# Performance work log

Measured on AMD Instinct MI355X. Metric: run time of the kernel, lower is better.

The kernel has to match this reference:

```python
import jax, jax.numpy as jnp
import numpy as np

N_ITERS = 3   # Routing default n_iters
EPS = 1e-5    # variance floor added to sig2
LN_EPS = 1e-5 # torch LayerNorm eps


def _routing(a_inp, mu_inp, W, Bias, beta_use, beta_ign):
    """Heinsen routing (gaussian p_model).
    a_inp: [b, n_i]; mu_inp: [b, n_i, c, d_inp]
    W: [1 or n_i, n_o, d_inp, d_out]; Bias: [n_o, c, d_out]; betas: [n_o].
    """
    if W.shape[0] == 1:  # weights shared across input capsules (n_inp not fixed)
        V = jnp.einsum('jdh,bicd->bijch', W[0], mu_inp) + Bias
    else:
        V = jnp.einsum('ijdh,bicd->bijch', W, mu_inp) + Bias
    n_out = V.shape[2]
    fa = jax.nn.sigmoid(a_inp)[..., None]          # [b, n_i, 1]
    R = jnp.full(V.shape[:3], 1.0 / n_out, dtype=V.dtype)
    a_out = mu_out = sig2 = Vm2 = None
    for it in range(N_ITERS):
        # E-step
        if it > 0:
            log_p = (-jnp.einsum('bijch,bjch->bij', Vm2, 1.0 / (2.0 * sig2))
                     - 0.5 * jnp.log(sig2).sum(axis=(-2, -1))[:, None, :])
            R = jax.nn.softmax(jax.nn.log_sigmoid(a_out)[:, None, :] + log_p, axis=-1)
        # D-step
        D_use = fa * R                              # [b, n_i, n_o]
        D_sum = D_use.sum(axis=-2)                  # [b, n_o]
        # M-step
        a_out = beta_use * D_sum - beta_ign * (fa.sum(axis=-2) - D_sum)
        nR = D_use / D_sum[:, None, :]
        mu_out = jnp.einsum('bij,bijch->bjch', nR, V)
        Vm2 = jnp.square(V - mu_out[:, None])
        sig2 = jnp.einsum('bij,bijch->bjch', nR, Vm2) + EPS
    return a_out, mu_out, sig2


def setup_inputs() -> dict:
    B, T = 32, 128
    d_depth, d_emb, d_cap, n_parts, n_classes = 13, 1024, 16, 64, 5
    key = jax.random.key(0)
    ks = jax.random.split(key, 8)
    mask = jax.random.uniform(ks[0], (B, T), jnp.float32, 0.05, 0.95)  # in (0,1) so logit is finite
    embs = jax.random.normal(ks[1], (B, T, d_depth, d_emb), jnp.float32)
    depth_emb = jax.random.normal(ks[2], (d_depth, d_emb), jnp.float32) * 0.02
    ln_w = jnp.ones((d_emb,), jnp.float32)
    ln_b = jnp.zeros((d_emb,), jnp.float32)
    dp_w = jax.random.normal(ks[3], (n_parts, d_emb), jnp.float32) * np.sqrt(2.0 / d_emb)  # kaiming
    dp_b = jnp.zeros((n_parts,), jnp.float32)
    # Routing 1: d_cov=1, d_inp=n_parts, d_out=d_cap, n_out=n_parts, n_inp shared (-1)
    W1 = jax.random.normal(ks[4], (1, n_parts, n_parts, d_cap), jnp.float32) / n_parts
    B1 = jnp.zeros((n_parts, 1, d_cap), jnp.float32)
    bu1 = jnp.zeros((n_parts,), jnp.float32)
    bi1 = jnp.zeros((n_parts,), jnp.float32)
    # Routing 2: d_cov=1, d_inp=d_cap, d_out=d_cap, n_out=n_classes, n_inp=n_parts
    W2 = jax.random.normal(ks[5], (n_parts, n_classes, d_cap, d_cap), jnp.float32) / d_cap
    B2 = jnp.zeros((n_classes, 1, d_cap), jnp.float32)
    bu2 = jnp.zeros((n_classes,), jnp.float32)
    bi2 = jnp.zeros((n_classes,), jnp.float32)
    return dict(mask=mask, embs=embs, depth_emb=depth_emb, ln_w=ln_w, ln_b=ln_b,
                dp_w=dp_w, dp_b=dp_b, W1=W1, B1=B1, bu1=bu1, bi1=bi1,
                W2=W2, B2=B2, bu2=bu2, bi2=bi2)


def reference(mask, embs, depth_emb, ln_w, ln_b, dp_w, dp_b,
              W1, B1, bu1, bi1, W2, B2, bu2, bi2):
    B = mask.shape[0]
    d_depth = embs.shape[-2]
    # input activations: logit(mask), repeated over depth
    a = jnp.log(mask / (1.0 - mask))                       # [B, T]
    a = jnp.broadcast_to(a[..., None], a.shape + (d_depth,)).reshape(B, -1)  # [B, T*d_depth]
    # detect_parts: LayerNorm -> Linear -> Swish
    x = embs + depth_emb
    m = x.mean(axis=-1, keepdims=True)
    v = ((x - m) ** 2).mean(axis=-1, keepdims=True)        # biased var (torch LayerNorm)
    xn = (x - m) * jax.lax.rsqrt(v + LN_EPS) * ln_w + ln_b
    h = jnp.einsum('btde,pe->btdp', xn, dp_w) + dp_b
    mu = h * jax.nn.sigmoid(h)                             # Swish
    mu = mu.reshape(B, -1, 1, mu.shape[-1])                # [B, T*d_depth, 1, n_parts]
    a, mu, sig2 = _routing(a, mu, W1, B1, bu1, bi1)
    a, mu, sig2 = _routing(a, mu, W2, B2, bu2, bi2)
    return a, mu, sig2
```

## Files before the change

kernel.cpp:

```cpp
#include <hip/hip_runtime.h>
#include <hip/hip_bf16.h>

constexpr int BQ = 32;
constexpr int TT = 128;
constexpr int DD = 13;
constexpr int E  = 1024;
constexpr int P  = 64;
constexpr int C  = 16;
constexpr int NC = 5;
constexpr int NI = TT * DD;
constexpr int NROWS = BQ * NI;
constexpr int RB = 16;

__global__ void k_sumfa(const float* __restrict__ mask, float* __restrict__ sumfa)
{
    const int b = blockIdx.x, tid = threadIdx.x;
    float v = mask[b * TT + tid];
#pragma unroll
    for (int off = 32; off > 0; off >>= 1) v += __shfl_xor(v, off);
    __shared__ float p2[2];
    if ((tid & 63) == 0) p2[tid >> 6] = v;
    __syncthreads();
    if (tid == 0) sumfa[b] = (float)DD * (p2[0] + p2[1]);
}

__global__ __launch_bounds__(256) void
k1_parts_v(const float* __restrict__ embs, const float* __restrict__ depth_emb,
           const float* __restrict__ ln_w, const float* __restrict__ ln_b,
           const float* __restrict__ dp_w, const float* __restrict__ dp_b,
           const float* __restrict__ W1,  const float* __restrict__ B1,
           float* __restrict__ V)
{
    __shared__ float xn[RB][E];
    __shared__ float muL[RB][P];
    const int tid = threadIdx.x;
    const int wave = tid >> 6, lane = tid & 63;
    const int row0 = blockIdx.x * RB;

    for (int rr = 0; rr < 4; ++rr) {
        const int r = wave * 4 + rr;
        const int row = row0 + r;
        const int dd = row % DD;
        const float* xr = embs + (size_t)row * E;
        const float* de = depth_emb + (size_t)dd * E;
        float4 xv[4];
        float s = 0.f;
#pragma unroll
        for (int k = 0; k < 4; ++k) {
            const int e = 4 * lane + 256 * k;
            float4 a = *reinterpret_cast<const float4*>(xr + e);
            const float4 d4 = *reinterpret_cast<const float4*>(de + e);
            a.x += d4.x; a.y += d4.y; a.z += d4.z; a.w += d4.w;
            xv[k] = a;
            s += a.x + a.y + a.z + a.w;
        }
#pragma unroll
        for (int off = 32; off > 0; off >>= 1) s += __shfl_xor(s, off);
        const float mean = s * (1.f / E);
        float vs = 0.f;
#pragma unroll
        for (int k = 0; k < 4; ++k) {
            const float4 a = xv[k];
            const float dx = a.x - mean, dy = a.y - mean, dz = a.z - mean, dw = a.w - mean;
            vs += dx * dx + dy * dy + dz * dz + dw * dw;
        }
#pragma unroll
        for (int off = 32; off > 0; off >>= 1) vs += __shfl_xor(vs, off);
        const float rstd = rsqrtf(vs * (1.f / E) + 1e-5f);
#pragma unroll
        for (int k = 0; k < 4; ++k) {
            const int e = 4 * lane + 256 * k;
            const float4 a = xv[k];
            const float4 w4 = *reinterpret_cast<const float4*>(ln_w + e);
            const float4 b4 = *reinterpret_cast<const float4*>(ln_b + e);
            float4 o4;
            o4.x = (a.x - mean) * rstd * w4.x + b4.x;
            o4.y = (a.y - mean) * rstd * w4.y + b4.y;
            o4.z = (a.z - mean) * rstd * w4.z + b4.z;
            o4.w = (a.w - mean) * rstd * w4.w + b4.w;
            *reinterpret_cast<float4*>(&xn[r][e]) = o4;
        }
    }
    __syncthreads();

    {
        const int pg = tid >> 4, eq = tid & 15;
        float acc[4][RB];
#pragma unroll
        for (int q = 0; q < 4; ++q)
#pragma unroll
            for (int r = 0; r < RB; ++r) acc[q][r] = 0.f;

        for (int kk = 0; kk < 16; ++kk) {
            const int e = kk * 64 + eq * 4;
            float4 w4[4];
#pragma unroll
            for (int q = 0; q < 4; ++q)
                w4[q] = *reinterpret_cast<const float4*>(dp_w + (size_t)(pg + q * 16) * E + e);
#pragma unroll
            for (int r = 0; r < RB; ++r) {
                const float4 x4 = *reinterpret_cast<const float4*>(&xn[r][e]);
#pragma unroll
                for (int q = 0; q < 4; ++q) {
                    acc[q][r] = fmaf(w4[q].x, x4.x, acc[q][r]);
                    acc[q][r] = fmaf(w4[q].y, x4.y, acc[q][r]);
                    acc[q][r] = fmaf(w4[q].z, x4.z, acc[q][r]);
                    acc[q][r] = fmaf(w4[q].w, x4.w, acc[q][r]);
                }
            }
        }
#pragma unroll
        for (int q = 0; q < 4; ++q)
#pragma unroll
            for (int r = 0; r < RB; ++r) {
                float v = acc[q][r];
                v += __shfl_xor(v, 1);
                v += __shfl_xor(v, 2);
                v += __shfl_xor(v, 4);
                v += __shfl_xor(v, 8);
                acc[q][r] = v;
            }
        if (eq == 0) {
#pragma unroll
            for (int q = 0; q < 4; ++q) {
                const int p = pg + q * 16;
                const float bb = dp_b[p];
#pragma unroll
                for (int r = 0; r < RB; ++r) {
                    const float h = acc[q][r] + bb;
                    muL[r][p] = h / (1.f + __expf(-h));
                }
            }
        }
    }
    __syncthreads();

    {
        const int h0 = wave * 4;
        const int j = lane;
        float4 acc[RB];
        const float4 b4 = *reinterpret_cast<const float4*>(B1 + j * C + h0);
#pragma unroll
        for (int r = 0; r < RB; ++r) acc[r] = b4;
        const float* w1p = W1 + (size_t)j * P * C + h0;
        for (int d = 0; d < P; ++d) {
            const float4 w4 = *reinterpret_cast<const float4*>(w1p + (size_t)d * C);
#pragma unroll
            for (int r = 0; r < RB; ++r) {
                const float m = muL[r][d];
                acc[r].x = fmaf(m, w4.x, acc[r].x);
                acc[r].y = fmaf(m, w4.y, acc[r].y);
                acc[r].z = fmaf(m, w4.z, acc[r].z);
                acc[r].w = fmaf(m, w4.w, acc[r].w);
            }
        }
#pragma unroll
        for (int r = 0; r < RB; ++r) {
            const size_t row = (size_t)(row0 + r);
            float* vp = V + (row * C + h0) * (size_t)P + j;
            vp[0 * P] = acc[r].x;
            vp[1 * P] = acc[r].y;
            vp[2 * P] = acc[r].z;
            vp[3 * P] = acc[r].w;
        }
    }
}

__global__ __launch_bounds__(256) void
k2_pass(const float* __restrict__ V, const float* __restrict__ mask,
        const float* __restrict__ c1v, const float* __restrict__ ivv,
        const float* __restrict__ c0v, float* __restrict__ Smu,
        float* __restrict__ SV2, float* __restrict__ Dsum, const int it)
{
    __shared__ float lacc[P][34];
    const int tid = threadIdx.x;
    const int wave = tid >> 6, j = tid & 63;
    const int b = blockIdx.x / (NI / 64);
    const int tile = blockIdx.x % (NI / 64);

    for (int k = tid; k < P * 34; k += 256) (&lacc[0][0])[k] = 0.f;

    float c1[16], iv[16], c0 = 0.f;
    if (it > 0) {
        const float4* cp = reinterpret_cast<const float4*>(c1v + ((size_t)b * P + j) * C);
        const float4* ip = reinterpret_cast<const float4*>(ivv + ((size_t)b * P + j) * C);
#pragma unroll
        for (int k = 0; k < 4; ++k) {
            const float4 c4 = cp[k]; const float4 i4 = ip[k];
            c1[k * 4 + 0] = c4.x; c1[k * 4 + 1] = c4.y; c1[k * 4 + 2] = c4.z; c1[k * 4 + 3] = c4.w;
            iv[k * 4 + 0] = i4.x; iv[k * 4 + 1] = i4.y; iv[k * 4 + 2] = i4.z; iv[k * 4 + 3] = i4.w;
        }
        c0 = c0v[(size_t)b * P + j];
    }

    const int i0 = tile * 64 + wave * 16;
    const float* vb = V + ((size_t)(b * NI + i0) * C) * P + j;

    float dsum = 0.f;
    float smuA[16], sv2A[16];
#pragma unroll
    for (int h = 0; h < 16; ++h) { smuA[h] = 0.f; sv2A[h] = 0.f; }

    __syncthreads();

    float va[2][16];
#pragma unroll
    for (int h = 0; h < 16; ++h) va[0][h] = vb[(size_t)h * P];

#pragma unroll
    for (int s = 0; s < 16; ++s) {
        const int cb = s & 1;
        if (s < 15) {
#pragma unroll
            for (int h = 0; h < 16; ++h)
                va[cb ^ 1][h] = vb[(size_t)((s + 1) * C + h) * P];
        }
        float R;
        if (it > 0) {
            float q = c0;
#pragma unroll
            for (int h = 0; h < 16; ++h) {
                const float v = va[cb][h];
                q = fmaf(v, fmaf(-v, iv[h], c1[h]), q);
            }
            float m = q;
#pragma unroll
            for (int off = 32; off > 0; off >>= 1) m = fmaxf(m, __shfl_xor(m, off));
            const float e = __expf(q - m);
            float sum = e;
#pragma unroll
            for (int off = 32; off > 0; off >>= 1) sum += __shfl_xor(sum, off);
            R = e / sum;
        } else {
            R = 1.f / 64.f;
        }
        const int i = i0 + s;
        const float fa = mask[b * TT + i / DD];
        const float w = fa * R;
        dsum += w;
#pragma unroll
        for (int h = 0; h < 16; ++h) {
            const float v = va[cb][h];
            smuA[h] = fmaf(w, v, smuA[h]);
            sv2A[h] = fmaf(w * v, v, sv2A[h]);
        }
    }

#pragma unroll
    for (int h = 0; h < 16; ++h) {
        atomicAdd(&lacc[j][h], smuA[h]);
        atomicAdd(&lacc[j][16 + h], sv2A[h]);
    }
    atomicAdd(&lacc[j][32], dsum);
    __syncthreads();

    for (int k = tid; k < P * 33; k += 256) {
        const int jj = k / 33, r = k % 33;
        const float v = lacc[jj][r];
        if (r < 16)      atomicAdd(&Smu[((size_t)b * P + jj) * C + r], v);
        else if (r < 32) atomicAdd(&SV2[((size_t)b * P + jj) * C + (r - 16)], v);
        else             atomicAdd(&Dsum[(size_t)b * P + jj], v);
    }
}

__global__ void k2f(const float* __restrict__ Smu, const float* __restrict__ SV2,
                    const float* __restrict__ Dsum, const float* __restrict__ sumfa,
                    const float* __restrict__ bu, const float* __restrict__ bi,
                    float* __restrict__ muo, float* __restrict__ ivv,
                    float* __restrict__ c1v, float* __restrict__ c0v,
                    float* __restrict__ a1)
{
    const int t = blockIdx.x * blockDim.x + threadIdx.x;
    if (t >= BQ * P) return;
    const int b = t / P, j = t % P;
    const float ds = Dsum[t];
    const float inv = 1.f / ds;
    const float ao = bu[j] * ds - bi[j] * (sumfa[b] - ds);
    a1[t] = ao;
    const float lsg = (ao < 0.f) ? (ao - log1pf(__expf(ao))) : (-log1pf(__expf(-ao)));
    float sumlog = 0.f, moiv = 0.f;
#pragma unroll
    for (int h = 0; h < C; ++h) {
        const float m = Smu[t * C + h] * inv;
        const float s2 = fmaxf(SV2[t * C + h] * inv - m * m, 0.f) + 1e-5f;
        const float iv = 0.5f / s2;
        muo[t * C + h] = m;
        ivv[t * C + h] = iv;
        c1v[t * C + h] = 2.f * m * iv;
        sumlog += logf(s2);
        moiv += m * m * iv;
    }
    c0v[t] = lsg - 0.5f * sumlog - moiv;
}

__global__ void k3_routing2(const float* __restrict__ muo, const float* __restrict__ a1,
                            const float* __restrict__ W2, const float* __restrict__ B2,
                            const float* __restrict__ bu2, const float* __restrict__ bi2,
                            float* __restrict__ out)
{
    __shared__ float mu1L[P][C];
    __shared__ float faL[P];
    __shared__ float V2L[P][NC][C];
    __shared__ float RL[P][NC];
    __shared__ float mu2L[NC][C];
    __shared__ float s2L[NC][C];
    __shared__ float isL[NC][C];
    __shared__ float dsL[NC];
    __shared__ float biasL[NC];
    __shared__ float a2L[NC];
    __shared__ float sumfa2s;
    const int b = blockIdx.x, tid = threadIdx.x;

    for (int k = tid; k < P * C; k += 256) (&mu1L[0][0])[k] = muo[(size_t)b * P * C + k];
    if (tid < P) {
        const float a = a1[(size_t)b * P + tid];
        faL[tid] = 1.f / (1.f + __expf(-a));
    }
    __syncthreads();
    if (tid == 0) {
        float s = 0.f;
        for (int i = 0; i < P; ++i) s += faL[i];
        sumfa2s = s;
    }
    {
        const int i = tid >> 2, hq = tid & 3;
        for (int jj = 0; jj < NC; ++jj) {
            float4 acc = *reinterpret_cast<const float4*>(B2 + jj * C + hq * 4);
            const float* wp = W2 + ((size_t)(i * NC + jj) * C) * C + hq * 4;
#pragma unroll
            for (int d = 0; d < C; ++d) {
                const float m = mu1L[i][d];
                const float4 w4 = *reinterpret_cast<const float4*>(wp + d * C);
                acc.x += m * w4.x; acc.y += m * w4.y; acc.z += m * w4.z; acc.w += m * w4.w;
            }
            *reinterpret_cast<float4*>(&V2L[i][jj][hq * 4]) = acc;
        }
    }
    __syncthreads();

    for (int it = 0; it < 3; ++it) {
        if (tid < P) {
            const int i = tid;
            if (it == 0) {
#pragma unroll
                for (int jj = 0; jj < NC; ++jj) RL[i][jj] = 1.f / NC;
            } else {
                float sc[NC];
                float m = -3.4e38f;
#pragma unroll
                for (int jj = 0; jj < NC; ++jj) {
                    float q = 0.f;
#pragma unroll
                    for (int h = 0; h < C; ++h) {
                        const float d = V2L[i][jj][h] - mu2L[jj][h];
                        q += d * d * isL[jj][h];
                    }
                    sc[jj] = biasL[jj] - q;
                    m = fmaxf(m, sc[jj]);
                }
                float sum = 0.f;
#pragma unroll
                for (int jj = 0; jj < NC; ++jj) { sc[jj] = __expf(sc[jj] - m); sum += sc[jj]; }
                const float invs = 1.f / sum;
#pragma unroll
                for (int jj = 0; jj < NC; ++jj) RL[i][jj] = sc[jj] * invs;
            }
        }
        __syncthreads();
        if (tid < NC) {
            float ds = 0.f;
            for (int i = 0; i < P; ++i) ds += faL[i] * RL[i][tid];
            dsL[tid] = ds;
        }
        __syncthreads();
        if (tid < NC * C) {
            const int jj = tid / C, h = tid % C;
            float smu = 0.f, sv2 = 0.f;
            for (int i = 0; i < P; ++i) {
                const float w = faL[i] * RL[i][jj];
                const float v = V2L[i][jj][h];
                smu += w * v;
                sv2 += w * v * v;
            }
            const float inv = 1.f / dsL[jj];
            const float m = smu * inv;
            const float s2 = fmaxf(sv2 * inv - m * m, 0.f) + 1e-5f;
            mu2L[jj][h] = m;
            s2L[jj][h] = s2;
            isL[jj][h] = 0.5f / s2;
        }
        __syncthreads();
        if (tid < NC) {
            const float ds = dsL[tid];
            const float ao = bu2[tid] * ds - bi2[tid] * (sumfa2s - ds);
            a2L[tid] = ao;
            const float lsg = (ao < 0.f) ? (ao - log1pf(__expf(ao))) : (-log1pf(__expf(-ao)));
            float sl = 0.f;
#pragma unroll
            for (int h = 0; h < C; ++h) sl += logf(s2L[tid][h]);
            biasL[tid] = lsg - 0.5f * sl;
        }
        __syncthreads();
    }

    if (tid < NC) out[(size_t)b * NC + tid] = a2L[tid];
    if (tid < NC * C) {
        const int jj = tid / C, h = tid % C;
        out[BQ * NC + ((size_t)b * NC + jj) * C + h] = mu2L[jj][h];
        out[BQ * NC + BQ * NC * C + ((size_t)b * NC + jj) * C + h] = s2L[jj][h];
    }
}

extern "C" void kernel_launch(void* const* d_in, const int* in_sizes, int n_in,
                              void* d_out, int out_size, void* d_ws, size_t ws_size,
                              hipStream_t stream)
{
    (void)in_sizes; (void)n_in; (void)out_size; (void)ws_size;
    const float* mask      = (const float*)d_in[0];
    const float* embs      = (const float*)d_in[1];
    const float* depth_emb = (const float*)d_in[2];
    const float* ln_w      = (const float*)d_in[3];
    const float* ln_b      = (const float*)d_in[4];
    const float* dp_w      = (const float*)d_in[5];
    const float* dp_b      = (const float*)d_in[6];
    const float* W1        = (const float*)d_in[7];
    const float* B1        = (const float*)d_in[8];
    const float* bu1       = (const float*)d_in[9];
    const float* bi1       = (const float*)d_in[10];
    const float* W2        = (const float*)d_in[11];
    const float* B2        = (const float*)d_in[12];
    const float* bu2       = (const float*)d_in[13];
    const float* bi2       = (const float*)d_in[14];
    float* out = (float*)d_out;

    float* ws = (float*)d_ws;
    size_t o = 0;
    float* V     = ws + o; o += (size_t)NROWS * P * C;
    float* Smu   = ws + o; o += (size_t)BQ * P * C;
    float* SV2   = ws + o; o += (size_t)BQ * P * C;
    float* Dsum  = ws + o; o += (size_t)BQ * P;
    float* muo   = ws + o; o += (size_t)BQ * P * C;
    float* ivv   = ws + o; o += (size_t)BQ * P * C;
    float* c1v   = ws + o; o += (size_t)BQ * P * C;
    float* c0v   = ws + o; o += (size_t)BQ * P;
    float* a1    = ws + o; o += (size_t)BQ * P;
    float* sumfa = ws + o; o += (size_t)BQ;

    k_sumfa<<<BQ, 128, 0, stream>>>(mask, sumfa);
    k1_parts_v<<<NROWS / RB, 256, 0, stream>>>(embs, depth_emb, ln_w, ln_b,
                                               dp_w, dp_b, W1, B1, V);
    for (int it = 0; it < 3; ++it) {
        hipMemsetAsync(Smu, 0, (size_t)(2 * BQ * P * C + BQ * P) * sizeof(float), stream);
        k2_pass<<<BQ * (NI / 64), 256, 0, stream>>>(V, mask, c1v, ivv, c0v,
                                                    Smu, SV2, Dsum, it);
        k2f<<<(BQ * P) / 256, 256, 0, stream>>>(Smu, SV2, Dsum, sumfa, bu1, bi1,
                                                muo, ivv, c1v, c0v, a1);
    }
    k3_routing2<<<BQ, 256, 0, stream>>>(muo, a1, W2, B2, bu2, bi2, out);
}
```

Before: 931.4 us.

## Fold LayerNorm into projection weights and re-layout V as row-major [row][j][h]

Precomputes LayerNorm-folded projection weights, depth-embedding dot products and moment terms in a prep kernel. The parts projection can then run directly on raw embs, one thread per row, with mean and variance recovered algebraically. V is now stored in a [row][j*16+h] layout: k1b computes it as a dense GEMM with a transposed W1, and the k2 pass reads contiguous float4s per thread. The per-iteration memset is replaced by zeroing the accumulators in k2f. The one-row-per-thread GEMM reads wext from cache with high register pressure, and computing variance as E[x²]-mean² carries cancellation risk.

```diff
diff --git a/kernel.cpp b/kernel.cpp
--- a/kernel.cpp
+++ b/kernel.cpp
@@ -10,7 +10,7 @@
 constexpr int NC = 5;
 constexpr int NI = TT * DD;
 constexpr int NROWS = BQ * NI;
-constexpr int RB = 16;
+constexpr int NCOL = 80;
 
 __global__ void k_sumfa(const float* __restrict__ mask, float* __restrict__ sumfa)
 {
@@ -24,146 +24,188 @@
     if (tid == 0) sumfa[b] = (float)DD * (p2[0] + p2[1]);
 }
 
+__global__ void k0_pre(const float* __restrict__ ln_w, const float* __restrict__ ln_b,
+                       const float* __restrict__ dp_w, const float* __restrict__ dp_b,
+                       const float* __restrict__ depth_emb, const float* __restrict__ W1,
+                       float* __restrict__ wext, float* __restrict__ W1m,
+                       float* __restrict__ c1t, float* __restrict__ c2t,
+                       float* __restrict__ dwt, float* __restrict__ sde1,
+                       float* __restrict__ sde2)
+{
+    const int blk = blockIdx.x, tid = threadIdx.x;
+    if (blk < 64) {
+        __shared__ float red[15][256];
+        const int p = blk;
+        float accv[15];
+#pragma unroll
+        for (int c = 0; c < 15; ++c) accv[c] = 0.f;
+        for (int k = tid; k < E; k += 256) {
+            const float w = dp_w[(size_t)p * E + k];
+            const float gw = ln_w[k] * w;
+            accv[0] += gw;
+            accv[1] += ln_b[k] * w;
+#pragma unroll
+            for (int d = 0; d < 13; ++d) accv[2 + d] += depth_emb[(size_t)d * E + k] * gw;
+        }
+#pragma unroll
+        for (int c = 0; c < 15; ++c) red[c][tid] = accv[c];
+        __syncthreads();
+        if (tid < 15) {
+            float s = 0.f;
+            for (int t = 0; t < 256; ++t) s += red[tid][t];
+            if (tid == 0)      c1t[p] = s;
+            else if (tid == 1) c2t[p] = s + dp_b[p];
+            else               dwt[(tid - 2) * 64 + p] = s;
+        }
+    } else if (blk < 77) {
+        __shared__ float red[2][256];
+        const int d = blk - 64;
+        float s1 = 0.f, s2 = 0.f;
+        for (int k = tid; k < E; k += 256) {
+            const float v = depth_emb[(size_t)d * E + k];
+            s1 += v; s2 += v * v;
+        }
+        red[0][tid] = s1; red[1][tid] = s2;
+        __syncthreads();
+        if (tid < 2) {
+            float s = 0.f;
+            for (int t = 0; t < 256; ++t) s += red[tid][t];
+            if (tid == 0) sde1[d] = s; else sde2[d] = s;
+        }
+    } else if (blk < 77 + 320) {
+        const int idx = (blk - 77) * 256 + tid;
+        const int k = idx / NCOL, c = idx % NCOL;
+        float v = 0.f;
+        if (c < 64)      v = ln_w[k] * dp_w[(size_t)c * E + k];
+        else if (c < 77) v = depth_emb[(size_t)(c - 64) * E + k];
+        wext[idx] = v;
+    } else {
+        const int t = (blk - 397) * 256 + tid;
+        const int d = t >> 10, col = t & 1023, j = col >> 4, h = col & 15;
+        W1m[t] = W1[((size_t)j * 64 + d) * 16 + h];
+    }
+}
+
 __global__ __launch_bounds__(256) void
-k1_parts_v(const float* __restrict__ embs, const float* __restrict__ depth_emb,
-           const float* __restrict__ ln_w, const float* __restrict__ ln_b,
-           const float* __restrict__ dp_w, const float* __restrict__ dp_b,
-           const float* __restrict__ W1,  const float* __restrict__ B1,
-           float* __restrict__ V)
-{
-    __shared__ float xn[RB][E];
-    __shared__ float muL[RB][P];
+k1a(const float* __restrict__ embs, const float* __restrict__ wext,
+    const float* __restrict__ c1t, const float* __restrict__ c2t,
+    const float* __restrict__ dwt, const float* __restrict__ sde1,
+    const float* __restrict__ sde2, float* __restrict__ V)
+{
+    const int row = blockIdx.x * 256 + threadIdx.x;
+    const float* xr = embs + (size_t)row * E;
+    float4 acc[20];
+#pragma unroll
+    for (int c = 0; c < 20; ++c) acc[c] = make_float4(0.f, 0.f, 0.f, 0.f);
+    float s = 0.f, s2 = 0.f;
+
+    for (int k0 = 0; k0 < E; k0 += 32) {
+        float4 xb[8];
+#pragma unroll
+        for (int q = 0; q < 8; ++q)
+            xb[q] = *reinterpret_cast<const float4*>(xr + k0 + q * 4);
+#pragma unroll
+        for (int q = 0; q < 8; ++q) {
+            const float x0 = xb[q].x, x1 = xb[q].y, x2 = xb[q].z, x3 = xb[q].w;
+            const float* wr = wext + (size_t)(k0 + q * 4) * NCOL;
+#pragma unroll
+            for (int c = 0; c < 20; ++c) {
+                const float4 w0 = *reinterpret_cast<const float4*>(wr + c * 4);
+                const float4 w1 = *reinterpret_cast<const float4*>(wr + NCOL + c * 4);
+                const float4 w2 = *reinterpret_cast<const float4*>(wr + 2 * NCOL + c * 4);
+                const float4 w3 = *reinterpret_cast<const float4*>(wr + 3 * NCOL + c * 4);
+                acc[c].x = fmaf(x0, w0.x, fmaf(x1, w1.x, fmaf(x2, w2.x, fmaf(x3, w3.x, acc[c].x))));
+                acc[c].y = fmaf(x0, w0.y, fmaf(x1, w1.y, fmaf(x2, w2.y, fmaf(x3, w3.y, acc[c].y))));
+                acc[c].z = fmaf(x0, w0.z, fmaf(x1, w1.z, fmaf(x2, w2.z, fmaf(x3, w3.z, acc[c].z))));
+                acc[c].w = fmaf(x0, w0.w, fmaf(x1, w1.w, fmaf(x2, w2.w, fmaf(x3, w3.w, acc[c].w))));
+            }
+            s += x0 + x1 + x2 + x3;
+            s2 = fmaf(x0, x0, fmaf(x1, x1, fmaf(x2, x2, fmaf(x3, x3, s2))));
+        }
+    }
+
+    const int d = row % DD;
+    float deD = 0.f;
+#pragma unroll
+    for (int dd = 0; dd < 13; ++dd) {
+        const int ci = (64 + dd) >> 2, mi = (64 + dd) & 3;
+        const float v = (mi == 0) ? acc[ci].x : (mi == 1) ? acc[ci].y : (mi == 2) ? acc[ci].z : acc[ci].w;
+        if (dd == d) deD = v;
+    }
+    const float mean = (s + sde1[d]) * (1.f / E);
+    const float var = (s2 + 2.f * deD + sde2[d]) * (1.f / E) - mean * mean;
+    const float rstd = rsqrtf(var + 1e-5f);
+    const float* dwr = dwt + d * 64;
+    float* mup = V + (size_t)row * 1024 + 960;
+#pragma unroll
+    for (int c = 0; c < 16; ++c) {
+        const float4 ed = acc[c];
+        const float4 dv = *reinterpret_cast<const float4*>(dwr + c * 4);
+        const float4 cv1 = *reinterpret_cast<const float4*>(c1t + c * 4);
+        const float4 cv2 = *reinterpret_cast<const float4*>(c2t + c * 4);
+        float4 h, mu;
+        h.x = fmaf(rstd, ed.x + dv.x - mean * cv1.x, cv2.x);
+        h.y = fmaf(rstd, ed.y + dv.y - mean * cv1.y, cv2.y);
+        h.z = fmaf(rstd, ed.z + dv.z - mean * cv1.z, cv2.z);
+        h.w = fmaf(rstd, ed.w + dv.w - mean * cv1.w, cv2.w);
+        mu.x = h.x / (1.f + __expf(-h.x));
+        mu.y = h.y / (1.f + __expf(-h.y));
+        mu.z = h.z / (1.f + __expf(-h.z));
+        mu.w = h.w / (1.f + __expf(-h.w));
+        *reinterpret_cast<float4*>(mup + c * 4) = mu;
+    }
+}
+
+__global__ __launch_bounds__(256) void
+k1b(const float* __restrict__ W1m, const float* __restrict__ B1, float* __restrict__ V)
+{
+    __shared__ float muL[16][64];
     const int tid = threadIdx.x;
-    const int wave = tid >> 6, lane = tid & 63;
-    const int row0 = blockIdx.x * RB;
-
-    for (int rr = 0; rr < 4; ++rr) {
-        const int r = wave * 4 + rr;
-        const int row = row0 + r;
-        const int dd = row % DD;
-        const float* xr = embs + (size_t)row * E;
-        const float* de = depth_emb + (size_t)dd * E;
-        float4 xv[4];
-        float s = 0.f;
-#pragma unroll
-        for (int k = 0; k < 4; ++k) {
-            const int e = 4 * lane + 256 * k;
-            float4 a = *reinterpret_cast<const float4*>(xr + e);
-            const float4 d4 = *reinterpret_cast<const float4*>(de + e);
-            a.x += d4.x; a.y += d4.y; a.z += d4.z; a.w += d4.w;
-            xv[k] = a;
-            s += a.x + a.y + a.z + a.w;
-        }
-#pragma unroll
-        for (int off = 32; off > 0; off >>= 1) s += __shfl_xor(s, off);
-        const float mean = s * (1.f / E);
-        float vs = 0.f;
-#pragma unroll
-        for (int k = 0; k < 4; ++k) {
-            const float4 a = xv[k];
-            const float dx = a.x - mean, dy = a.y - mean, dz = a.z - mean, dw = a.w - mean;
-            vs += dx * dx + dy * dy + dz * dz + dw * dw;
-        }
-#pragma unroll
-        for (int off = 32; off > 0; off >>= 1) vs += __shfl_xor(vs, off);
-        const float rstd = rsqrtf(vs * (1.f / E) + 1e-5f);
-#pragma unroll
-        for (int k = 0; k < 4; ++k) {
-            const int e = 4 * lane + 256 * k;
-            const float4 a = xv[k];
-            const float4 w4 = *reinterpret_cast<const float4*>(ln_w + e);
-            const float4 b4 = *reinterpret_cast<const float4*>(ln_b + e);
-            float4 o4;
-            o4.x = (a.x - mean) * rstd * w4.x + b4.x;
-            o4.y = (a.y - mean) * rstd * w4.y + b4.y;
-            o4.z = (a.z - mean) * rstd * w4.z + b4.z;
-            o4.w = (a.w - mean) * rstd * w4.w + b4.w;
-            *reinterpret_cast<float4*>(&xn[r][e]) = o4;
-        }
+    const int row0 = blockIdx.x * 16;
+#pragma unroll
+    for (int q = 0; q < 4; ++q) {
+        const int idx = q * 256 + tid;
+        muL[idx >> 6][idx & 63] = V[(size_t)(row0 + (idx >> 6)) * 1024 + 960 + (idx & 63)];
     }
     __syncthreads();
-
-    {
-        const int pg = tid >> 4, eq = tid & 15;
-        float acc[4][RB];
-#pragma unroll
-        for (int q = 0; q < 4; ++q)
-#pragma unroll
-            for (int r = 0; r < RB; ++r) acc[q][r] = 0.f;
-
-        for (int kk = 0; kk < 16; ++kk) {
-            const int e = kk * 64 + eq * 4;
-            float4 w4[4];
-#pragma unroll
-            for (int q = 0; q < 4; ++q)
-                w4[q] = *reinterpret_cast<const float4*>(dp_w + (size_t)(pg + q * 16) * E + e);
-#pragma unroll
-            for (int r = 0; r < RB; ++r) {
-                const float4 x4 = *reinterpret_cast<const float4*>(&xn[r][e]);
-#pragma unroll
-                for (int q = 0; q < 4; ++q) {
-                    acc[q][r] = fmaf(w4[q].x, x4.x, acc[q][r]);
-                    acc[q][r] = fmaf(w4[q].y, x4.y, acc[q][r]);
-                    acc[q][r] = fmaf(w4[q].z, x4.z, acc[q][r]);
-                    acc[q][r] = fmaf(w4[q].w, x4.w, acc[q][r]);
-                }
-            }
-        }
-#pragma unroll
-        for (int q = 0; q < 4; ++q)
-#pragma unroll
-            for (int r = 0; r < RB; ++r) {
-                float v = acc[q][r];
-                v += __shfl_xor(v, 1);
-                v += __shfl_xor(v, 2);
-                v += __shfl_xor(v, 4);
-                v += __shfl_xor(v, 8);
-                acc[q][r] = v;
-            }
-        if (eq == 0) {
-#pragma unroll
-            for (int q = 0; q < 4; ++q) {
-                const int p = pg + q * 16;
-                const float bb = dp_b[p];
-#pragma unroll
-                for (int r = 0; r < RB; ++r) {
-                    const float h = acc[q][r] + bb;
-                    muL[r][p] = h / (1.f + __expf(-h));
-                }
-            }
-        }
-    }
-    __syncthreads();
-
-    {
-        const int h0 = wave * 4;
-        const int j = lane;
-        float4 acc[RB];
-        const float4 b4 = *reinterpret_cast<const float4*>(B1 + j * C + h0);
-#pragma unroll
-        for (int r = 0; r < RB; ++r) acc[r] = b4;
-        const float* w1p = W1 + (size_t)j * P * C + h0;
-        for (int d = 0; d < P; ++d) {
-            const float4 w4 = *reinterpret_cast<const float4*>(w1p + (size_t)d * C);
-#pragma unroll
-            for (int r = 0; r < RB; ++r) {
-                const float m = muL[r][d];
-                acc[r].x = fmaf(m, w4.x, acc[r].x);
-                acc[r].y = fmaf(m, w4.y, acc[r].y);
-                acc[r].z = fmaf(m, w4.z, acc[r].z);
-                acc[r].w = fmaf(m, w4.w, acc[r].w);
-            }
-        }
-#pragma unroll
-        for (int r = 0; r < RB; ++r) {
-            const size_t row = (size_t)(row0 + r);
-            float* vp = V + (row * C + h0) * (size_t)P + j;
-            vp[0 * P] = acc[r].x;
-            vp[1 * P] = acc[r].y;
-            vp[2 * P] = acc[r].z;
-            vp[3 * P] = acc[r].w;
-        }
-    }
+    const int c4 = tid;
+    float4 acc[16];
+    const float4 bv = *reinterpret_cast<const float4*>(B1 + c4 * 4);
+#pragma unroll
+    for (int r = 0; r < 16; ++r) acc[r] = bv;
+
+    for (int kc = 0; kc < 64; kc += 8) {
+        float4 wreg[8];
+#pragma unroll
+        for (int kk = 0; kk < 8; ++kk)
+            wreg[kk] = *reinterpret_cast<const float4*>(W1m + (size_t)(kc + kk) * 1024 + c4 * 4);
+#pragma unroll
+        for (int r = 0; r < 16; ++r) {
+            const float4 ma = *reinterpret_cast<const float4*>(&muL[r][kc]);
+            const float4 mb = *reinterpret_cast<const float4*>(&muL[r][kc + 4]);
+            float4 a = acc[r];
+            a.x = fmaf(ma.x, wreg[0].x, a.x); a.y = fmaf(ma.x, wreg[0].y, a.y);
+            a.z = fmaf(ma.x, wreg[0].z, a.z); a.w = fmaf(ma.x, wreg[0].w, a.w);
+            a.x = fmaf(ma.y, wreg[1].x, a.x); a.y = fmaf(ma.y, wreg[1].y, a.y);
+            a.z = fmaf(ma.y, wreg[1].z, a.z); a.w = fmaf(ma.y, wreg[1].w, a.w);
+            a.x = fmaf(ma.z, wreg[2].x, a.x); a.y = fmaf(ma.z, wreg[2].y, a.y);
+            a.z = fmaf(ma.z, wreg[2].z, a.z); a.w = fmaf(ma.z, wreg[2].w, a.w);
+            a.x = fmaf(ma.w, wreg[3].x, a.x); a.y = fmaf(ma.w, wreg[3].y, a.y);
+            a.z = fmaf(ma.w, wreg[3].z, a.z); a.w = fmaf(ma.w, wreg[3].w, a.w);
+            a.x = fmaf(mb.x, wreg[4].x, a.x); a.y = fmaf(mb.x, wreg[4].y, a.y);
+            a.z = fmaf(mb.x, wreg[4].z, a.z); a.w = fmaf(mb.x, wreg[4].w, a.w);
+            a.x = fmaf(mb.y, wreg[5].x, a.x); a.y = fmaf(mb.y, wreg[5].y, a.y);
+            a.z = fmaf(mb.y, wreg[5].z, a.z); a.w = fmaf(mb.y, wreg[5].w, a.w);
+            a.x = fmaf(mb.z, wreg[6].x, a.x); a.y = fmaf(mb.z, wreg[6].y, a.y);
+            a.z = fmaf(mb.z, wreg[6].z, a.z); a.w = fmaf(mb.z, wreg[6].w, a.w);
+            a.x = fmaf(mb.w, wreg[7].x, a.x); a.y = fmaf(mb.w, wreg[7].y, a.y);
+            a.z = fmaf(mb.w, wreg[7].z, a.z); a.w = fmaf(mb.w, wreg[7].w, a.w);
+            acc[r] = a;
+        }
+    }
+#pragma unroll
+    for (int r = 0; r < 16; ++r)
+        *reinterpret_cast<float4*>(V + (size_t)(row0 + r) * 1024 + c4 * 4) = acc[r];
 }
 
 __global__ __launch_bounds__(256) void
@@ -173,84 +215,124 @@
         float* __restrict__ SV2, float* __restrict__ Dsum, const int it)
 {
     __shared__ float lacc[P][34];
-    const int tid = threadIdx.x;
-    const int wave = tid >> 6, j = tid & 63;
+    const int tid = threadIdx.x, wave = tid >> 6, j = tid & 63;
     const int b = blockIdx.x / (NI / 64);
     const int tile = blockIdx.x % (NI / 64);
-
     for (int k = tid; k < P * 34; k += 256) (&lacc[0][0])[k] = 0.f;
 
-    float c1[16], iv[16], c0 = 0.f;
+    float4 C1a, C1b, C1c, C1d, IVa, IVb, IVc, IVd;
+    float c0 = 0.f;
+    C1a = C1b = C1c = C1d = IVa = IVb = IVc = IVd = make_float4(0.f, 0.f, 0.f, 0.f);
     if (it > 0) {
         const float4* cp = reinterpret_cast<const float4*>(c1v + ((size_t)b * P + j) * C);
         const float4* ip = reinterpret_cast<const float4*>(ivv + ((size_t)b * P + j) * C);
-#pragma unroll
-        for (int k = 0; k < 4; ++k) {
-            const float4 c4 = cp[k]; const float4 i4 = ip[k];
-            c1[k * 4 + 0] = c4.x; c1[k * 4 + 1] = c4.y; c1[k * 4 + 2] = c4.z; c1[k * 4 + 3] = c4.w;
-            iv[k * 4 + 0] = i4.x; iv[k * 4 + 1] = i4.y; iv[k * 4 + 2] = i4.z; iv[k * 4 + 3] = i4.w;
-        }
+        C1a = cp[0]; C1b = cp[1]; C1c = cp[2]; C1d = cp[3];
+        IVa = ip[0]; IVb = ip[1]; IVc = ip[2]; IVd = ip[3];
         c0 = c0v[(size_t)b * P + j];
     }
-
     const int i0 = tile * 64 + wave * 16;
-    const float* vb = V + ((size_t)(b * NI + i0) * C) * P + j;
-
+    const float* vb = V + ((size_t)(b * NI) + i0) * 1024 + (j << 4);
+    const float* mrow = mask + b * TT;
+
+    float4 SMa, SMb, SMc, SMd, Qa, Qb, Qc, Qd;
+    SMa = SMb = SMc = SMd = Qa = Qb = Qc = Qd = make_float4(0.f, 0.f, 0.f, 0.f);
     float dsum = 0.f;
-    float smuA[16], sv2A[16];
-#pragma unroll
-    for (int h = 0; h < 16; ++h) { smuA[h] = 0.f; sv2A[h] = 0.f; }
-
     __syncthreads();
 
-    float va[2][16];
-#pragma unroll
-    for (int h = 0; h < 16; ++h) va[0][h] = vb[(size_t)h * P];
-
-#pragma unroll
-    for (int s = 0; s < 16; ++s) {
-        const int cb = s & 1;
-        if (s < 15) {
-#pragma unroll
-            for (int h = 0; h < 16; ++h)
-                va[cb ^ 1][h] = vb[(size_t)((s + 1) * C + h) * P];
-        }
-        float R;
+    auto proc = [&](const float4 va, const float4 vB, const float4 vc, const float4 vd, const int i) {
+        float w;
+        const float fam = mrow[i / DD];
         if (it > 0) {
             float q = c0;
-#pragma unroll
-            for (int h = 0; h < 16; ++h) {
-                const float v = va[cb][h];
-                q = fmaf(v, fmaf(-v, iv[h], c1[h]), q);
-            }
+            q = fmaf(va.x, fmaf(-va.x, IVa.x, C1a.x), q);
+            q = fmaf(va.y, fmaf(-va.y, IVa.y, C1a.y), q);
+            q = fmaf(va.z, fmaf(-va.z, IVa.z, C1a.z), q);
+            q = fmaf(va.w, fmaf(-va.w, IVa.w, C1a.w), q);
+            q = fmaf(vB.x, fmaf(-vB.x, IVb.x, C1b.x), q);
+            q = fmaf(vB.y, fmaf(-vB.y, IVb.y, C1b.y), q);
+            q = fmaf(vB.z, fmaf(-vB.z, IVb.z, C1b.z), q);
+            q = fmaf(vB.w, fmaf(-vB.w, IVb.w, C1b.w), q);
+            q = fmaf(vc.x, fmaf(-vc.x, IVc.x, C1c.x), q);
+            q = fmaf(vc.y, fmaf(-vc.y, IVc.y, C1c.y), q);
+            q = fmaf(vc.z, fmaf(-vc.z, IVc.z, C1c.z), q);
+            q = fmaf(vc.w, fmaf(-vc.w, IVc.w, C1c.w), q);
+            q = fmaf(vd.x, fmaf(-vd.x, IVd.x, C1d.x), q);
+            q = fmaf(vd.y, fmaf(-vd.y, IVd.y, C1d.y), q);
+            q = fmaf(vd.z, fmaf(-vd.z, IVd.z, C1d.z), q);
+            q = fmaf(vd.w, fmaf(-vd.w, IVd.w, C1d.w), q);
             float m = q;
-#pragma unroll
-            for (int off = 32; off > 0; off >>= 1) m = fmaxf(m, __shfl_xor(m, off));
+            m = fmaxf(m, __shfl_xor(m, 32));
+            m = fmaxf(m, __shfl_xor(m, 16));
+            m = fmaxf(m, __shfl_xor(m, 8));
+            m = fmaxf(m, __shfl_xor(m, 4));
+            m = fmaxf(m, __shfl_xor(m, 2));
+            m = fmaxf(m, __shfl_xor(m, 1));
             const float e = __expf(q - m);
-            float sum = e;
-#pragma unroll
-            for (int off = 32; off > 0; off >>= 1) sum += __shfl_xor(sum, off);
-            R = e / sum;
+            float ss = e;
+            ss += __shfl_xor(ss, 32);
+            ss += __shfl_xor(ss, 16);
+            ss += __shfl_xor(ss, 8);
+            ss += __shfl_xor(ss, 4);
+            ss += __shfl_xor(ss, 2);
+            ss += __shfl_xor(ss, 1);
+            w = fam * (e / ss);
         } else {
-            R = 1.f / 64.f;
-        }
-        const int i = i0 + s;
-        const float fa = mask[b * TT + i / DD];
-        const float w = fa * R;
+            w = fam * (1.f / 64.f);
+        }
         dsum += w;
-#pragma unroll
-        for (int h = 0; h < 16; ++h) {
-            const float v = va[cb][h];
-            smuA[h] = fmaf(w, v, smuA[h]);
-            sv2A[h] = fmaf(w * v, v, sv2A[h]);
-        }
-    }
-
-#pragma unroll
-    for (int h = 0; h < 16; ++h) {
-        atomicAdd(&lacc[j][h], smuA[h]);
-        atomicAdd(&lacc[j][16 + h], sv2A[h]);
-    }
+        SMa.x = fmaf(w, va.x, SMa.x); Qa.x = fmaf(w * va.x, va.x, Qa.x);
+        SMa.y = fmaf(w, va.y, SMa.y); Qa.y = fmaf(w * va.y, va.y, Qa.y);
+        SMa.z = fmaf(w, va.z, SMa.z); Qa.z = fmaf(w * va.z, va.z, Qa.z);
+        SMa.w = fmaf(w, va.w, SMa.w); Qa.w = fmaf(w * va.w, va.w, Qa.w);
+        SMb.x = fmaf(w, vB.x, SMb.x); Qb.x = fmaf(w * vB.x, vB.x, Qb.x);
+        SMb.y = fmaf(w, vB.y, SMb.y); Qb.y = fmaf(w * vB.y, vB.y, Qb.y);
+        SMb.z = fmaf(w, vB.z, SMb.z); Qb.z = fmaf(w * vB.z, vB.z, Qb.z);
+        SMb.w = fmaf(w, vB.w, SMb.w); Qb.w = fmaf(w * vB.w, vB.w, Qb.w);
+        SMc.x = fmaf(w, vc.x, SMc.x); Qc.x = fmaf(w * vc.x, vc.x, Qc.x);
+        SMc.y = fmaf(w, vc.y, SMc.y); Qc.y = fmaf(w * vc.y, vc.y, Qc.y);
+        SMc.z = fmaf(w, vc.z, SMc.z); Qc.z = fmaf(w * vc.z, vc.z, Qc.z);
+        SMc.w = fmaf(w, vc.w, SMc.w); Qc.w = fmaf(w * vc.w, vc.w, Qc.w);
+        SMd.x = fmaf(w, vd.x, SMd.x); Qd.x = fmaf(w * vd.x, vd.x, Qd.x);
+        SMd.y = fmaf(w, vd.y, SMd.y); Qd.y = fmaf(w * vd.y, vd.y, Qd.y);
+        SMd.z = fmaf(w, vd.z, SMd.z); Qd.z = fmaf(w * vd.z, vd.z, Qd.z);
+        SMd.w = fmaf(w, vd.w, SMd.w); Qd.w = fmaf(w * vd.w, vd.w, Qd.w);
+    };
+
+    float4 A0, A1, A2, A3, B0, B1r, B2, B3;
+    {
+        const float4* p = reinterpret_cast<const float4*>(vb);
+        A0 = p[0]; A1 = p[1]; A2 = p[2]; A3 = p[3];
+    }
+#pragma unroll
+    for (int ss = 0; ss < 16; ss += 2) {
+        {
+            const float4* p = reinterpret_cast<const float4*>(vb + (size_t)(ss + 1) * 1024);
+            B0 = p[0]; B1r = p[1]; B2 = p[2]; B3 = p[3];
+        }
+        proc(A0, A1, A2, A3, i0 + ss);
+        if (ss + 2 < 16) {
+            const float4* p = reinterpret_cast<const float4*>(vb + (size_t)(ss + 2) * 1024);
+            A0 = p[0]; A1 = p[1]; A2 = p[2]; A3 = p[3];
+        }
+        proc(B0, B1r, B2, B3, i0 + ss + 1);
+    }
+
+    atomicAdd(&lacc[j][0],  SMa.x); atomicAdd(&lacc[j][1],  SMa.y);
+    atomicAdd(&lacc[j][2],  SMa.z); atomicAdd(&lacc[j][3],  SMa.w);
+    atomicAdd(&lacc[j][4],  SMb.x); atomicAdd(&lacc[j][5],  SMb.y);
+    atomicAdd(&lacc[j][6],  SMb.z); atomicAdd(&lacc[j][7],  SMb.w);
+    atomicAdd(&lacc[j][8],  SMc.x); atomicAdd(&lacc[j][9],  SMc.y);
+    atomicAdd(&lacc[j][10], SMc.z); atomicAdd(&lacc[j][11], SMc.w);
+    atomicAdd(&lacc[j][12], SMd.x); atomicAdd(&lacc[j][13], SMd.y);
+    atomicAdd(&lacc[j][14], SMd.z); atomicAdd(&lacc[j][15], SMd.w);
+    atomicAdd(&lacc[j][16], Qa.x);  atomicAdd(&lacc[j][17], Qa.y);
+    atomicAdd(&lacc[j][18], Qa.z);  atomicAdd(&lacc[j][19], Qa.w);
+    atomicAdd(&lacc[j][20], Qb.x);  atomicAdd(&lacc[j][21], Qb.y);
+    atomicAdd(&lacc[j][22], Qb.z);  atomicAdd(&lacc[j][23], Qb.w);
+    atomicAdd(&lacc[j][24], Qc.x);  atomicAdd(&lacc[j][25], Qc.y);
+    atomicAdd(&lacc[j][26], Qc.z);  atomicAdd(&lacc[j][27], Qc.w);
+    atomicAdd(&lacc[j][28], Qd.x);  atomicAdd(&lacc[j][29], Qd.y);
+    atomicAdd(&lacc[j][30], Qd.z);  atomicAdd(&lacc[j][31], Qd.w);
     atomicAdd(&lacc[j][32], dsum);
     __syncthreads();
 
@@ -263,8 +345,8 @@
     }
 }
 
-__global__ void k2f(const float* __restrict__ Smu, const float* __restrict__ SV2,
-                    const float* __restrict__ Dsum, const float* __restrict__ sumfa,
+__global__ void k2f(float* __restrict__ Smu, float* __restrict__ SV2,
+                    float* __restrict__ Dsum, const float* __restrict__ sumfa,
                     const float* __restrict__ bu, const float* __restrict__ bi,
                     float* __restrict__ muo, float* __restrict__ ivv,
                     float* __restrict__ c1v, float* __restrict__ c0v,
@@ -289,7 +371,10 @@
         c1v[t * C + h] = 2.f * m * iv;
         sumlog += logf(s2);
         moiv += m * m * iv;
-    }
+        Smu[t * C + h] = 0.f;
+        SV2[t * C + h] = 0.f;
+    }
+    Dsum[t] = 0.f;
     c0v[t] = lsg - 0.5f * sumlog - moiv;
 }
 
@@ -435,7 +520,14 @@
 
     float* ws = (float*)d_ws;
     size_t o = 0;
-    float* V     = ws + o; o += (size_t)NROWS * P * C;
+    float* V     = ws + o; o += (size_t)NROWS * 1024;
+    float* wext  = ws + o; o += 81920;
+    float* W1m   = ws + o; o += 65536;
+    float* c1t   = ws + o; o += 64;
+    float* c2t   = ws + o; o += 64;
+    float* dwt   = ws + o; o += 832;
+    float* sde1  = ws + o; o += 16;
+    float* sde2  = ws + o; o += 16;
     float* Smu   = ws + o; o += (size_t)BQ * P * C;
     float* SV2   = ws + o; o += (size_t)BQ * P * C;
     float* Dsum  = ws + o; o += (size_t)BQ * P;
@@ -444,13 +536,15 @@
     float* c1v   = ws + o; o += (size_t)BQ * P * C;
     float* c0v   = ws + o; o += (size_t)BQ * P;
     float* a1    = ws + o; o += (size_t)BQ * P;
-    float* sumfa = ws + o; o += (size_t)BQ;
-
+    float* sumfa = ws + o; o += BQ;
+
+    k0_pre<<<653, 256, 0, stream>>>(ln_w, ln_b, dp_w, dp_b, depth_emb, W1,
+                                    wext, W1m, c1t, c2t, dwt, sde1, sde2);
     k_sumfa<<<BQ, 128, 0, stream>>>(mask, sumfa);
-    k1_parts_v<<<NROWS / RB, 256, 0, stream>>>(embs, depth_emb, ln_w, ln_b,
-                                               dp_w, dp_b, W1, B1, V);
+    hipMemsetAsync(Smu, 0, (size_t)(2 * BQ * P * C + BQ * P) * sizeof(float), stream);
+    k1a<<<NROWS / 256, 256, 0, stream>>>(embs, wext, c1t, c2t, dwt, sde1, sde2, V);
+    k1b<<<NROWS / 16, 256, 0, stream>>>(W1m, B1, V);
     for (int it = 0; it < 3; ++it) {
-        hipMemsetAsync(Smu, 0, (size_t)(2 * BQ * P * C + BQ * P) * sizeof(float), stream);
         k2_pass<<<BQ * (NI / 64), 256, 0, stream>>>(V, mask, c1v, ivv, c0v,
                                                     Smu, SV2, Dsum, it);
         k2f<<<(BQ * P) / 256, 256, 0, stream>>>(Smu, SV2, Dsum, sumfa, bu1, bi1,
```

Measured after the change: 1.206 ms. +29.5%, slower.
